# Kernel tuning notes

Hardware: AMD Instinct MI355X
Metric: run time of the kernel (lower is better)

## Reference

```python
import jax, jax.numpy as jnp
import numpy as np

B, C, H, W = 8, 64, 48, 48
W_SCALE = 0.05  # ~1/sqrt(fan_in=128)


def conv1x1(x, w, b):
    # x: [B, Cin, H, W], w: [Cout, Cin], b: [Cout]
    return jnp.einsum('oc,bchw->bohw', w, x) + b[None, :, None, None]


def setup_inputs() -> dict:
    key = jax.random.key(0)
    ks = jax.random.split(key, 12)
    n = lambda k, s, sc=1.0: jax.random.normal(k, s, dtype=jnp.float32) * sc
    return {
        'xlh': n(ks[0], (B, C, H, W)),
        'xll': n(ks[1], (B, C, H, W)),
        'xrh': n(ks[2], (B, C, H, W)),
        'xrl': n(ks[3], (B, C, H, W)),
        'concaL_w': n(ks[4], (C, 2 * C), W_SCALE), 'concaL_b': jnp.zeros((C,), jnp.float32),
        'concaR_w': n(ks[5], (C, 2 * C), W_SCALE), 'concaR_b': jnp.zeros((C,), jnp.float32),
        'gateL_w': n(ks[6], (1, C), W_SCALE), 'gateL_b': jnp.zeros((1,), jnp.float32),
        'gateR_w': n(ks[7], (1, C), W_SCALE), 'gateR_b': jnp.zeros((1,), jnp.float32),
        'concaLo_w': n(ks[8], (C, 2 * C), W_SCALE), 'concaLo_b': jnp.zeros((C,), jnp.float32),
        'concaRo_w': n(ks[9], (C, 2 * C), W_SCALE), 'concaRo_b': jnp.zeros((C,), jnp.float32),
    }


def reference(xlh, xll, xrh, xrl,
              concaL_w, concaL_b, concaR_w, concaR_b,
              gateL_w, gateL_b, gateR_w, gateR_b,
              concaLo_w, concaLo_b, concaRo_w, concaRo_b):
    xL = conv1x1(jnp.concatenate([xlh, xll], axis=1), concaL_w, concaL_b)  # [B,C,H,W]
    xR = conv1x1(jnp.concatenate([xrh, xrl], axis=1), concaR_w, concaR_b)
    bs, ch, hei, wei = xL.shape
    hw = hei * wei
    xLr = xL.reshape(bs, ch, hw)  # [B,C,HW]
    xRr = xR.reshape(bs, ch, hw)
    # Affinity = xL^T xR : [B, HW_L, HW_R]
    aff = jnp.einsum('bcn,bcm->bnm', xLr, xRr)
    a1 = jax.nn.softmax(aff, axis=1)  # softmax over left positions
    a2 = jax.nn.softmax(aff, axis=2)  # softmax over right positions
    # Branch1: xL @ a1 -> [B,C,HW]
    b1 = jnp.einsum('bcn,bnm->bcm', xLr, a1).reshape(bs, ch, hei, wei)
    g1 = jax.nn.sigmoid(conv1x1(b1, gateL_w, gateL_b))  # [B,1,H,W]
    b1 = b1 * g1
    # Branch2: xR @ a2 -> [B,C,HW]
    b2 = jnp.einsum('bcn,bnm->bcm', xRr, a2).reshape(bs, ch, hei, wei)
    g2 = jax.nn.sigmoid(conv1x1(b2, gateR_w, gateR_b))
    b2 = b2 * g2
    out_L = conv1x1(jnp.concatenate([xL, b1], axis=1), concaLo_w, concaLo_b)
    out_R = conv1x1(jnp.concatenate([xR, b2], axis=1), concaRo_w, concaRo_b)
    return (out_L, out_R)
```

## Files before the change

### kernel.cpp

```cpp
#include <hip/hip_runtime.h>

typedef unsigned short u16;
typedef __bf16 bf16_t;
typedef bf16_t bf16x8 __attribute__((ext_vector_type(8)));
typedef float f32x4 __attribute__((ext_vector_type(4)));

#define B_   8
#define CH   64
#define HW   2304
#define L2E  1.4426950408889634f

#define OFF_XLC   0u
#define OFF_XRC   2359296u
#define OFF_XLT   4718592u
#define OFF_XRT   7077888u
#define OFF_B1    9437184u
#define OFF_B2    14155776u
#define OFF_RS2   18874368u

__device__ __forceinline__ float bf2f(u16 u){
  union { unsigned int i; float f; } v; v.i = ((unsigned int)u) << 16; return v.f;
}
__device__ __forceinline__ u16 f2bf(float f){
  union { float f; unsigned int i; } v; v.f = f;
  unsigned int r = v.i + 0x7FFFu + ((v.i >> 16) & 1u);
  return (u16)(r >> 16);
}
__device__ __forceinline__ void gload16(const void* g, void* l){
  __builtin_amdgcn_global_load_lds(
      (const __attribute__((address_space(1))) void*)g,
      (__attribute__((address_space(3))) void*)l, 16, 0, 0);
}

__global__ __launch_bounds__(256) void k_proj(
    const float* xlh, const float* xll, const float* xrh, const float* xrl,
    const float* wLl, const float* bLl, const float* wRr, const float* bRr,
    char* ws)
{
  int bid = blockIdx.x;
  int b   = bid & 7;
  int q   = bid >> 3;
  int o0  = (q & 3) * 16;
  int side= (q >> 2) & 1;
  int p   = (q >> 3) * 256 + threadIdx.x;
  const float* xh = (side ? xrh : xlh) + (size_t)b*CH*HW;
  const float* xl = (side ? xrl : xll) + (size_t)b*CH*HW;
  const float* w  = (side ? wRr : wLl);
  const float* bi = (side ? bRr : bLl);

  float acc[16];
  #pragma unroll
  for (int j=0;j<16;j++) acc[j] = bi[o0+j];
  for (int c=0;c<64;c++){
    float xv = xh[(size_t)c*HW + p];
    #pragma unroll
    for (int j=0;j<16;j++) acc[j] = fmaf(w[(size_t)(o0+j)*128 + c], xv, acc[j]);
  }
  for (int c=0;c<64;c++){
    float xv = xl[(size_t)c*HW + p];
    #pragma unroll
    for (int j=0;j<16;j++) acc[j] = fmaf(w[(size_t)(o0+j)*128 + 64 + c], xv, acc[j]);
  }
  u16* xc = (u16*)(ws + (side ? OFF_XRC : OFF_XLC)) + (size_t)b*CH*HW;
  u16* xt = (u16*)(ws + (side ? OFF_XRT : OFF_XLT)) + (size_t)b*HW*CH;
  unsigned int pk[8];
  #pragma unroll
  for (int j=0;j<8;j++){
    unsigned int lo16 = f2bf(acc[2*j]);
    unsigned int hi16 = f2bf(acc[2*j+1]);
    pk[j] = lo16 | (hi16 << 16);
    xc[(size_t)(o0+2*j  )*HW + p] = (u16)lo16;
    xc[(size_t)(o0+2*j+1)*HW + p] = (u16)hi16;
  }
  uint4* dst = (uint4*)&xt[(size_t)p*CH + o0];
  dst[0] = make_uint4(pk[0],pk[1],pk[2],pk[3]);
  dst[1] = make_uint4(pk[4],pk[5],pk[6],pk[7]);
}

__global__ __launch_bounds__(256, 4) void k_stats(char* ws)
{
  __shared__ alignas(16) char smraw[16384];
  __shared__ float part[4][2][4][4];
  int bid = blockIdx.x;
  int b   = bid & 7;
  int r0  = (bid >> 3) * 32;
  const char* Xb = ws + OFF_XLT + (size_t)b*HW*CH*2;
  const char* Yb = ws + OFF_XRT + (size_t)b*HW*CH*2;
  float* out = (float*)(ws + OFF_RS2) + b*HW;

  int lane = threadIdx.x & 63;
  int wv   = __builtin_amdgcn_readfirstlane(threadIdx.x >> 6);
  int lo = lane & 15, g = lane >> 4;
  int l = lane;

  const u16* Xu = (const u16*)Xb;
  bf16x8 aA0 = *(const bf16x8*)&Xu[(size_t)(r0+lo)*CH + 8*g];
  bf16x8 aA1 = *(const bf16x8*)&Xu[(size_t)(r0+lo)*CH + 32 + 8*g];
  bf16x8 aB0 = *(const bf16x8*)&Xu[(size_t)(r0+16+lo)*CH + 8*g];
  bf16x8 aB1 = *(const bf16x8*)&Xu[(size_t)(r0+16+lo)*CH + 32 + 8*g];

  int ySrc[2];
  #pragma unroll
  for (int j=0;j<2;j++){
    int r = j*8 + (l>>3);
    ySrc[j] = r*128 + (((l&7) ^ (r&7)))*16;
  }
  char* myY = smraw + wv*4096;
  int jbP = wv*576, jbQ = jbP + 288;

  int rdP0 = lo*128 + ((g      ^ (lo&7)))*16;
  int rdP1 = lo*128 + (((4|g)  ^ (lo&7)))*16;

  #define STAGE_S(i) do { \
    const char* gp = Yb + (size_t)(jbP + (i)*16)*128; \
    const char* gq = Yb + (size_t)(jbQ + (i)*16)*128; \
    gload16(gp + ySrc[0], myY + 0);    gload16(gp + ySrc[1], myY + 1024); \
    gload16(gq + ySrc[0], myY + 2048); gload16(gq + ySrc[1], myY + 3072); \
  } while(0)

  float sPA[4] = {0.f,0.f,0.f,0.f};
  float sQA[4] = {0.f,0.f,0.f,0.f};
  float sPB[4] = {0.f,0.f,0.f,0.f};
  float sQB[4] = {0.f,0.f,0.f,0.f};

  STAGE_S(0);
  for (int i = 0; i < 18; ++i){
    asm volatile("s_waitcnt vmcnt(0)" ::: "memory");
    __builtin_amdgcn_sched_barrier(0);
    bf16x8 bP0 = *(const bf16x8*)(myY + rdP0);
    bf16x8 bP1 = *(const bf16x8*)(myY + rdP1);
    bf16x8 bQ0 = *(const bf16x8*)(myY + 2048 + rdP0);
    bf16x8 bQ1 = *(const bf16x8*)(myY + 2048 + rdP1);
    asm volatile("s_waitcnt lgkmcnt(0)" ::: "memory");
    __builtin_amdgcn_sched_barrier(0);
    int inext = (i+1 < 18) ? i+1 : 0;
    STAGE_S(inext);
    __builtin_amdgcn_sched_barrier(0);
    f32x4 z4 = {0.f,0.f,0.f,0.f};
    f32x4 dPA = __builtin_amdgcn_mfma_f32_16x16x32_bf16(aA0, bP0, z4, 0,0,0);
    dPA = __builtin_amdgcn_mfma_f32_16x16x32_bf16(aA1, bP1, dPA, 0,0,0);
    f32x4 dQA = __builtin_amdgcn_mfma_f32_16x16x32_bf16(aA0, bQ0, z4, 0,0,0);
    dQA = __builtin_amdgcn_mfma_f32_16x16x32_bf16(aA1, bQ1, dQA, 0,0,0);
    f32x4 dPB = __builtin_amdgcn_mfma_f32_16x16x32_bf16(aB0, bP0, z4, 0,0,0);
    dPB = __builtin_amdgcn_mfma_f32_16x16x32_bf16(aB1, bP1, dPB, 0,0,0);
    f32x4 dQB = __builtin_amdgcn_mfma_f32_16x16x32_bf16(aB0, bQ0, z4, 0,0,0);
    dQB = __builtin_amdgcn_mfma_f32_16x16x32_bf16(aB1, bQ1, dQB, 0,0,0);
    #pragma unroll
    for (int r=0;r<4;r++){
      sPA[r] += exp2f(dPA[r]*L2E); sQA[r] += exp2f(dQA[r]*L2E);
      sPB[r] += exp2f(dPB[r]*L2E); sQB[r] += exp2f(dQB[r]*L2E);
    }
  }
  #undef STAGE_S
  float sA[4], sB[4];
  #pragma unroll
  for (int r=0;r<4;r++){ sA[r] = sPA[r] + sQA[r]; sB[r] = sPB[r] + sQB[r]; }
  #pragma unroll
  for (int mask = 1; mask < 16; mask <<= 1){
    #pragma unroll
    for (int r=0;r<4;r++){
      sA[r] += __shfl_xor(sA[r], mask, 64);
      sB[r] += __shfl_xor(sB[r], mask, 64);
    }
  }
  if (lo == 0){
    #pragma unroll
    for (int r=0;r<4;r++){ part[wv][0][g][r] = sA[r]; part[wv][1][g][r] = sB[r]; }
  }
  __syncthreads();
  if (threadIdx.x < 32){
    int t = threadIdx.x;
    int half = t >> 4, gg = (t & 15) >> 2, rr = t & 3;
    float sum = part[0][half][gg][rr] + part[1][half][gg][rr]
              + part[2][half][gg][rr] + part[3][half][gg][rr];
    out[r0 + 16*half + 4*gg + rr] = 1.0f / sum;
  }
}

__global__ __launch_bounds__(256, 3) void k_attn(char* ws)
{
  __shared__ alignas(16) char smraw[49152];
  int bid  = blockIdx.x;
  int b    = bid & 7;
  int m0   = (bid >> 3) * 32;
  int lane = threadIdx.x & 63;
  int wv   = __builtin_amdgcn_readfirstlane(threadIdx.x >> 6);
  int lo = lane & 15, g = lane >> 4;
  int l = lane;

  const char* XLt = ws + OFF_XLT + (size_t)b*HW*CH*2;
  const char* XRt = ws + OFF_XRT + (size_t)b*HW*CH*2;
  const char* XLc = ws + OFF_XLC + (size_t)b*CH*HW*2;
  const char* XRc = ws + OFF_XRC + (size_t)b*CH*HW*2;
  const float* rs2 = (const float*)(ws + OFF_RS2) + b*HW;

  const u16* XRtu = (const u16*)XRt;
  bf16x8 fmA0 = *(const bf16x8*)&XRtu[(size_t)(m0+lo)*CH + 8*g];
  bf16x8 fmA1 = *(const bf16x8*)&XRtu[(size_t)(m0+lo)*CH + 32 + 8*g];
  bf16x8 fmB0 = *(const bf16x8*)&XRtu[(size_t)(m0+16+lo)*CH + 8*g];
  bf16x8 fmB1 = *(const bf16x8*)&XRtu[(size_t)(m0+16+lo)*CH + 32 + 8*g];

  int aSrc[4], bSrc[4];
  #pragma unroll
  for (int j=0;j<4;j++){
    int r  = j*8 + (l>>3);
    int sa = (r&3) | (((r>>3)&1)<<2);
    aSrc[j] = r*128 + (((l&7) ^ sa))*16;
    int c  = j*16 + (l>>2);
    int sb = (c>>1)&3;
    bSrc[j] = c*(HW*2) + (((l&3) ^ sb))*16;
  }
  char* myA  = smraw + wv*12288;
  char* myBL = myA + 4096;
  char* myBR = myA + 8192;

  int pr  = ((lo>>2)<<3) + (lo&3);
  int sAr = (lo&3) | (((lo>>2)&1)<<2);
  int rdA00 = pr*128     + ((g     ^ sAr))*16;
  int rdA01 = pr*128     + (((4|g) ^ sAr))*16;
  int rdA10 = (pr+4)*128 + ((g     ^ sAr))*16;
  int rdA11 = (pr+4)*128 + (((4|g) ^ sAr))*16;
  int sBr = (lo>>1)&3;
  int rdB0 = (     lo)*64 + ((g ^ sBr))*16;
  int rdB1 = (16 + lo)*64 + ((g ^ sBr))*16;
  int rdB2 = (32 + lo)*64 + ((g ^ sBr))*16;
  int rdB3 = (48 + lo)*64 + ((g ^ sBr))*16;

  #define STAGE_A(n0v) do { \
    const char* gA = XLt + (size_t)(n0v)*128; \
    const char* gL = XLc + (size_t)(n0v)*2; \
    const char* gR = XRc + (size_t)(n0v)*2; \
    gload16(gA + aSrc[0], myA  + 0);    gload16(gA + aSrc[1], myA  + 1024); \
    gload16(gA + aSrc[2], myA  + 2048); gload16(gA + aSrc[3], myA  + 3072); \
    gload16(gL + bSrc[0], myBL + 0);    gload16(gL + bSrc[1], myBL + 1024); \
    gload16(gL + bSrc[2], myBL + 2048); gload16(gL + bSrc[3], myBL + 3072); \
    gload16(gR + bSrc[0], myBR + 0);    gload16(gR + bSrc[1], myBR + 1024); \
    gload16(gR + bSrc[2], myBR + 2048); gload16(gR + bSrc[3], myBR + 3072); \
  } while(0)

  f32x4 acc1A[4], acc2A[4], acc1B[4], acc2B[4];
  #pragma unroll
  for (int ct=0;ct<4;ct++){
    f32x4 z4 = {0.f,0.f,0.f,0.f};
    acc1A[ct]=z4; acc2A[ct]=z4; acc1B[ct]=z4; acc2B[ct]=z4;
  }
  float s1A = 0.f, s1B = 0.f;

  int nbeg = wv * 576;
  STAGE_A(nbeg);
  for (int s = 0; s < 18; ++s){
    int n0 = nbeg + s*32;
    asm volatile("s_waitcnt vmcnt(0)" ::: "memory");
    __builtin_amdgcn_sched_barrier(0);
    bf16x8 fa00 = *(const bf16x8*)(myA + rdA00);
    bf16x8 fa01 = *(const bf16x8*)(myA + rdA01);
    bf16x8 fa10 = *(const bf16x8*)(myA + rdA10);
    bf16x8 fa11 = *(const bf16x8*)(myA + rdA11);
    bf16x8 bL0 = *(const bf16x8*)(myBL + rdB0);
    bf16x8 bL1 = *(const bf16x8*)(myBL + rdB1);
    bf16x8 bL2 = *(const bf16x8*)(myBL + rdB2);
    bf16x8 bL3 = *(const bf16x8*)(myBL + rdB3);
    bf16x8 bR0 = *(const bf16x8*)(myBR + rdB0);
    bf16x8 bR1 = *(const bf16x8*)(myBR + rdB1);
    bf16x8 bR2 = *(const bf16x8*)(myBR + rdB2);
    bf16x8 bR3 = *(const bf16x8*)(myBR + rdB3);
    f32x4 r20 = *(const f32x4*)&rs2[n0 + 8*g];
    f32x4 r21 = *(const f32x4*)&rs2[n0 + 8*g + 4];
    asm volatile("s_waitcnt lgkmcnt(0)" ::: "memory");
    __builtin_amdgcn_sched_barrier(0);
    int n1 = (s+1 < 18) ? n0 + 32 : nbeg;
    STAGE_A(n1);
    __builtin_amdgcn_sched_barrier(0);

    f32x4 z4 = {0.f,0.f,0.f,0.f};
    f32x4 d0A = __builtin_amdgcn_mfma_f32_16x16x32_bf16(fa00, fmA0, z4, 0,0,0);
    d0A = __builtin_amdgcn_mfma_f32_16x16x32_bf16(fa01, fmA1, d0A, 0,0,0);
    f32x4 d1A = __builtin_amdgcn_mfma_f32_16x16x32_bf16(fa10, fmA0, z4, 0,0,0);
    d1A = __builtin_amdgcn_mfma_f32_16x16x32_bf16(fa11, fmA1, d1A, 0,0,0);
    f32x4 d0B = __builtin_amdgcn_mfma_f32_16x16x32_bf16(fa00, fmB0, z4, 0,0,0);
    d0B = __builtin_amdgcn_mfma_f32_16x16x32_bf16(fa01, fmB1, d0B, 0,0,0);
    f32x4 d1B = __builtin_amdgcn_mfma_f32_16x16x32_bf16(fa10, fmB0, z4, 0,0,0);
    d1B = __builtin_amdgcn_mfma_f32_16x16x32_bf16(fa11, fmB1, d1B, 0,0,0);

    bf16x8 pa1A, pa2A, pa1B, pa2B;
    #pragma unroll
    for (int r=0;r<4;r++){
      float e0 = exp2f(d0A[r]*L2E);
      float e1 = exp2f(d1A[r]*L2E);
      s1A += e0 + e1;
      pa1A[r]   = (bf16_t)e0;
      pa1A[r+4] = (bf16_t)e1;
      pa2A[r]   = (bf16_t)(e0 * r20[r]);
      pa2A[r+4] = (bf16_t)(e1 * r21[r]);
      float f0 = exp2f(d0B[r]*L2E);
      float f1 = exp2f(d1B[r]*L2E);
      s1B += f0 + f1;
      pa1B[r]   = (bf16_t)f0;
      pa1B[r+4] = (bf16_t)f1;
      pa2B[r]   = (bf16_t)(f0 * r20[r]);
      pa2B[r+4] = (bf16_t)(f1 * r21[r]);
    }
    acc1A[0] = __builtin_amdgcn_mfma_f32_16x16x32_bf16(pa1A, bL0, acc1A[0], 0,0,0);
    acc1A[1] = __builtin_amdgcn_mfma_f32_16x16x32_bf16(pa1A, bL1, acc1A[1], 0,0,0);
    acc1A[2] = __builtin_amdgcn_mfma_f32_16x16x32_bf16(pa1A, bL2, acc1A[2], 0,0,0);
    acc1A[3] = __builtin_amdgcn_mfma_f32_16x16x32_bf16(pa1A, bL3, acc1A[3], 0,0,0);
    acc2A[0] = __builtin_amdgcn_mfma_f32_16x16x32_bf16(pa2A, bR0, acc2A[0], 0,0,0);
    acc2A[1] = __builtin_amdgcn_mfma_f32_16x16x32_bf16(pa2A, bR1, acc2A[1], 0,0,0);
    acc2A[2] = __builtin_amdgcn_mfma_f32_16x16x32_bf16(pa2A, bR2, acc2A[2], 0,0,0);
    acc2A[3] = __builtin_amdgcn_mfma_f32_16x16x32_bf16(pa2A, bR3, acc2A[3], 0,0,0);
    acc1B[0] = __builtin_amdgcn_mfma_f32_16x16x32_bf16(pa1B, bL0, acc1B[0], 0,0,0);
    acc1B[1] = __builtin_amdgcn_mfma_f32_16x16x32_bf16(pa1B, bL1, acc1B[1], 0,0,0);
    acc1B[2] = __builtin_amdgcn_mfma_f32_16x16x32_bf16(pa1B, bL2, acc1B[2], 0,0,0);
    acc1B[3] = __builtin_amdgcn_mfma_f32_16x16x32_bf16(pa1B, bL3, acc1B[3], 0,0,0);
    acc2B[0] = __builtin_amdgcn_mfma_f32_16x16x32_bf16(pa2B, bR0, acc2B[0], 0,0,0);
    acc2B[1] = __builtin_amdgcn_mfma_f32_16x16x32_bf16(pa2B, bR1, acc2B[1], 0,0,0);
    acc2B[2] = __builtin_amdgcn_mfma_f32_16x16x32_bf16(pa2B, bR2, acc2B[2], 0,0,0);
    acc2B[3] = __builtin_amdgcn_mfma_f32_16x16x32_bf16(pa2B, bR3, acc2B[3], 0,0,0);
  }
  #undef STAGE_A

  asm volatile("s_waitcnt vmcnt(0)" ::: "memory");
  __syncthreads();

  float (*red)[64][17] = (float (*)[64][17])smraw;
  float (*s1part)[32]  = (float (*)[32])(smraw + 17408);
  float* rs1inv        = (float*)(smraw + 17920);

  float s1Ar = s1A + __shfl_xor(s1A, 16, 64);
  s1Ar += __shfl_xor(s1Ar, 32, 64);
  float s1Br = s1B + __shfl_xor(s1B, 16, 64);
  s1Br += __shfl_xor(s1Br, 32, 64);
  if (lane < 16){ s1part[wv][lane] = s1Ar; s1part[wv][16+lane] = s1Br; }
  __syncthreads();
  if (threadIdx.x < 32){
    int t = threadIdx.x;
    float s = s1part[0][t] + s1part[1][t] + s1part[2][t] + s1part[3][t];
    rs1inv[t] = 1.0f / s;
  }
  __syncthreads();

  float* B1 = (float*)(ws + OFF_B1) + (size_t)b*CH*HW;
  float* B2 = (float*)(ws + OFF_B2) + (size_t)b*CH*HW;
  int tt = threadIdx.x;

  #define RED_WRITE(DST, MBASE, SCALE) do { \
    _Pragma("unroll") \
    for (int pass=0; pass<4; ++pass){ \
      int c  = (tt>>4) + pass*16; \
      int mm = tt & 15; \
      int v  = ((c>>4)<<2) + (mm&3); \
      int ll = (c&15) + ((mm>>2)<<4); \
      float s = red[0][ll][v] + red[1][ll][v] + red[2][ll][v] + red[3][ll][v]; \
      DST[(size_t)c*HW + m0 + (MBASE) + mm] = s * (SCALE); \
    } \
  } while(0)

  #pragma unroll
  for (int v=0; v<16; ++v) red[wv][lane][v] = acc1A[v>>2][v&3];
  __syncthreads();
  RED_WRITE(B1, 0, rs1inv[tt & 15]);
  __syncthreads();
  #pragma unroll
  for (int v=0; v<16; ++v) red[wv][lane][v] = acc2A[v>>2][v&3];
  __syncthreads();
  RED_WRITE(B2, 0, 1.0f);
  __syncthreads();
  #pragma unroll
  for (int v=0; v<16; ++v) red[wv][lane][v] = acc1B[v>>2][v&3];
  __syncthreads();
  RED_WRITE(B1, 16, rs1inv[16 + (tt & 15)]);
  __syncthreads();
  #pragma unroll
  for (int v=0; v<16; ++v) red[wv][lane][v] = acc2B[v>>2][v&3];
  __syncthreads();
  RED_WRITE(B2, 16, 1.0f);
  #undef RED_WRITE
}

__global__ __launch_bounds__(256) void k_out(
    char* ws,
    const float* gwL, const float* gbL, const float* gwR, const float* gbR,
    const float* wLo, const float* bLoi, const float* wRo, const float* bRoi,
    float* out)
{
  __shared__ float xT[64][64];
  __shared__ float bT[64][64];
  __shared__ float gpart[4][64];
  __shared__ float gLds[64];
  int bid = blockIdx.x;
  int b   = bid & 7;
  int q   = bid >> 3;
  int side= q & 1;
  int p0  = (q >> 1) * 64;
  int t = threadIdx.x;
  const float* braw = (const float*)(ws + (side ? OFF_B2 : OFF_B1)) + (size_t)b*CH*HW;
  const u16*   xc   = (const u16*)(ws + (side ? OFF_XRC : OFF_XLC)) + (size_t)b*CH*HW;
  const float* w    = side ? wRo : wLo;
  const float* gw   = side ? gwR : gwL;
  float        gb   = side ? gbR[0] : gbL[0];
  const float* bias = side ? bRoi : bLoi;

  #pragma unroll
  for (int i=0;i<16;i++){
    int flat = i*256 + t;
    int c = flat >> 6, pl = flat & 63;
    bT[c][pl] = braw[(size_t)c*HW + p0 + pl];
    xT[c][pl] = bf2f(xc[(size_t)c*HW + p0 + pl]);
  }
  __syncthreads();
  {
    int qq = t >> 6, pl = t & 63;
    float a = 0.f;
    #pragma unroll
    for (int c = 0; c < 16; c++) a = fmaf(gw[16*qq + c], bT[16*qq + c][pl], a);
    gpart[qq][pl] = a;
  }
  __syncthreads();
  if (t < 64){
    float x = gpart[0][t]+gpart[1][t]+gpart[2][t]+gpart[3][t] + gb;
    gLds[t] = 1.0f/(1.0f + exp2f(-x*L2E));
  }
  __syncthreads();
  #pragma unroll
  for (int i=0;i<16;i++){
    int flat = i*256 + t;
    int c = flat >> 6, pl = flat & 63;
    bT[c][pl] *= gLds[pl];
  }
  __syncthreads();
  int wv = t >> 6;
  int lane = t & 63;
  float* outp = out + ((size_t)side*B_ + b)*CH*HW;

  float acc[16];
  #pragma unroll
  for (int oi=0;oi<16;oi++) acc[oi] = bias[wv*16 + oi];
  for (int c=0;c<64;c++){
    float xv = xT[c][lane];
    float bv = bT[c][lane];
    #pragma unroll
    for (int oi=0;oi<16;oi++){
      int o = wv*16 + oi;
      acc[oi] = fmaf(w[(size_t)o*128 + c],      xv, acc[oi]);
      acc[oi] = fmaf(w[(size_t)o*128 + 64 + c], bv, acc[oi]);
    }
  }
  #pragma unroll
  for (int oi=0;oi<16;oi++){
    int o = wv*16 + oi;
    outp[(size_t)o*HW + p0 + lane] = acc[oi];
  }
}

extern "C" void kernel_launch(void* const* d_in, const int* in_sizes, int n_in,
                              void* d_out, int out_size, void* d_ws, size_t ws_size,
                              hipStream_t stream)
{
  char* ws = (char*)d_ws;
  k_proj <<<576, 256, 0, stream>>>(
      (const float*)d_in[0], (const float*)d_in[1],
      (const float*)d_in[2], (const float*)d_in[3],
      (const float*)d_in[4], (const float*)d_in[5],
      (const float*)d_in[6], (const float*)d_in[7], ws);
  k_stats<<<576, 256, 0, stream>>>(ws);
  k_attn <<<576, 256, 0, stream>>>(ws);
  k_out  <<<576, 256, 0, stream>>>(
      ws,
      (const float*)d_in[8],  (const float*)d_in[9],
      (const float*)d_in[10], (const float*)d_in[11],
      (const float*)d_in[12], (const float*)d_in[13],
      (const float*)d_in[14], (const float*)d_in[15],
      (float*)d_out);
}
```

Measured before the change: 158.7 us.

## Fuse gating and output projection into attention kernel epilogue

The separate k_out kernel is folded into the end of k_attn. The reduced branch outputs (b1, b2) now stay in shared memory instead of being written to and re-read from the workspace as fp32. The epilogue loads the matching xL/xR bf16 tile, computes the sigmoid gates, and runs both 1x1 output convolutions per 32-position tile, splitting the channels across half-waves that are combined with a shuffle. This removes one launch and the fp32 round-trip of B1/B2. In exchange the attention kernel's tail gets longer and heavier in registers: each thread holds 64 floats and reads weights scalar-per-lane, the gate dot product runs on only 64 threads, and occupancy may suffer.

```diff
diff --git a/kernel.cpp b/kernel.cpp
--- a/kernel.cpp
+++ b/kernel.cpp
@@ -14,8 +14,6 @@
 #define OFF_XRC   2359296u
 #define OFF_XLT   4718592u
 #define OFF_XRT   7077888u
-#define OFF_B1    9437184u
-#define OFF_B2    14155776u
 #define OFF_RS2   18874368u
 
 __device__ __forceinline__ float bf2f(u16 u){
@@ -177,7 +175,11 @@
   }
 }
 
-__global__ __launch_bounds__(256, 3) void k_attn(char* ws)
+__global__ __launch_bounds__(256, 3) void k_attn(
+    char* ws,
+    const float* gwL, const float* gbL, const float* gwR, const float* gbR,
+    const float* wLo, const float* bLo, const float* wRo, const float* bRo,
+    float* outp)
 {
   __shared__ alignas(16) char smraw[49152];
   int bid  = blockIdx.x;
@@ -322,9 +324,26 @@
   asm volatile("s_waitcnt vmcnt(0)" ::: "memory");
   __syncthreads();
 
-  float (*red)[64][17] = (float (*)[64][17])smraw;
-  float (*s1part)[32]  = (float (*)[32])(smraw + 17408);
-  float* rs1inv        = (float*)(smraw + 17920);
+  float (*bT1)[33]     = (float (*)[33])smraw;
+  float (*bT2)[33]     = (float (*)[33])(smraw + 8448);
+  float (*red)[64][17] = (float (*)[64][17])(smraw + 16896);
+  u16   (*xT1)[34]     = (u16 (*)[34])(smraw + 34304);
+  u16   (*xT2)[34]     = (u16 (*)[34])(smraw + 38656);
+  float (*s1part)[32]  = (float (*)[32])(smraw + 43008);
+  float* rs1inv        = (float*)(smraw + 43520);
+  float* gate          = (float*)(smraw + 43648);
+
+  int tt = threadIdx.x;
+
+  const u16* XLcu = (const u16*)XLc;
+  const u16* XRcu = (const u16*)XRc;
+  #pragma unroll
+  for (int i=0;i<8;i++){
+    int flat = i*256 + tt;
+    int c = flat >> 5, mm = flat & 31;
+    xT1[c][mm] = XLcu[(size_t)c*HW + m0 + mm];
+    xT2[c][mm] = XRcu[(size_t)c*HW + m0 + mm];
+  }
 
   float s1Ar = s1A + __shfl_xor(s1A, 16, 64);
   s1Ar += __shfl_xor(s1Ar, 32, 64);
@@ -332,18 +351,13 @@
   s1Br += __shfl_xor(s1Br, 32, 64);
   if (lane < 16){ s1part[wv][lane] = s1Ar; s1part[wv][16+lane] = s1Br; }
   __syncthreads();
-  if (threadIdx.x < 32){
-    int t = threadIdx.x;
-    float s = s1part[0][t] + s1part[1][t] + s1part[2][t] + s1part[3][t];
-    rs1inv[t] = 1.0f / s;
-  }
-  __syncthreads();
-
-  float* B1 = (float*)(ws + OFF_B1) + (size_t)b*CH*HW;
-  float* B2 = (float*)(ws + OFF_B2) + (size_t)b*CH*HW;
-  int tt = threadIdx.x;
-
-  #define RED_WRITE(DST, MBASE, SCALE) do { \
+  if (tt < 32){
+    float s = s1part[0][tt] + s1part[1][tt] + s1part[2][tt] + s1part[3][tt];
+    rs1inv[tt] = 1.0f / s;
+  }
+  __syncthreads();
+
+  #define RED_TO(DSTARR, MBASE, SCALED) do { \
     _Pragma("unroll") \
     for (int pass=0; pass<4; ++pass){ \
       int c  = (tt>>4) + pass*16; \
@@ -351,104 +365,81 @@
       int v  = ((c>>4)<<2) + (mm&3); \
       int ll = (c&15) + ((mm>>2)<<4); \
       float s = red[0][ll][v] + red[1][ll][v] + red[2][ll][v] + red[3][ll][v]; \
-      DST[(size_t)c*HW + m0 + (MBASE) + mm] = s * (SCALE); \
+      DSTARR[c][(MBASE)+mm] = (SCALED) ? s * rs1inv[(MBASE)+mm] : s; \
     } \
   } while(0)
 
   #pragma unroll
   for (int v=0; v<16; ++v) red[wv][lane][v] = acc1A[v>>2][v&3];
   __syncthreads();
-  RED_WRITE(B1, 0, rs1inv[tt & 15]);
+  RED_TO(bT1, 0, 1);
   __syncthreads();
   #pragma unroll
   for (int v=0; v<16; ++v) red[wv][lane][v] = acc2A[v>>2][v&3];
   __syncthreads();
-  RED_WRITE(B2, 0, 1.0f);
+  RED_TO(bT2, 0, 0);
   __syncthreads();
   #pragma unroll
   for (int v=0; v<16; ++v) red[wv][lane][v] = acc1B[v>>2][v&3];
   __syncthreads();
-  RED_WRITE(B1, 16, rs1inv[16 + (tt & 15)]);
+  RED_TO(bT1, 16, 1);
   __syncthreads();
   #pragma unroll
   for (int v=0; v<16; ++v) red[wv][lane][v] = acc2B[v>>2][v&3];
   __syncthreads();
-  RED_WRITE(B2, 16, 1.0f);
-  #undef RED_WRITE
-}
-
-__global__ __launch_bounds__(256) void k_out(
-    char* ws,
-    const float* gwL, const float* gbL, const float* gwR, const float* gbR,
-    const float* wLo, const float* bLoi, const float* wRo, const float* bRoi,
-    float* out)
-{
-  __shared__ float xT[64][64];
-  __shared__ float bT[64][64];
-  __shared__ float gpart[4][64];
-  __shared__ float gLds[64];
-  int bid = blockIdx.x;
-  int b   = bid & 7;
-  int q   = bid >> 3;
-  int side= q & 1;
-  int p0  = (q >> 1) * 64;
-  int t = threadIdx.x;
-  const float* braw = (const float*)(ws + (side ? OFF_B2 : OFF_B1)) + (size_t)b*CH*HW;
-  const u16*   xc   = (const u16*)(ws + (side ? OFF_XRC : OFF_XLC)) + (size_t)b*CH*HW;
-  const float* w    = side ? wRo : wLo;
-  const float* gw   = side ? gwR : gwL;
-  float        gb   = side ? gbR[0] : gbL[0];
-  const float* bias = side ? bRoi : bLoi;
-
-  #pragma unroll
-  for (int i=0;i<16;i++){
-    int flat = i*256 + t;
-    int c = flat >> 6, pl = flat & 63;
-    bT[c][pl] = braw[(size_t)c*HW + p0 + pl];
-    xT[c][pl] = bf2f(xc[(size_t)c*HW + p0 + pl]);
-  }
-  __syncthreads();
+  RED_TO(bT2, 16, 0);
+  #undef RED_TO
+  __syncthreads();
+
+  if (tt < 64){
+    int mm = tt & 31;
+    float a = 0.f;
+    if (tt < 32){
+      for (int c=0;c<64;c++) a = fmaf(gwL[c], bT1[c][mm], a);
+      gate[tt] = 1.0f/(1.0f + exp2f(-(a + gbL[0])*L2E));
+    } else {
+      for (int c=0;c<64;c++) a = fmaf(gwR[c], bT2[c][mm], a);
+      gate[tt] = 1.0f/(1.0f + exp2f(-(a + gbR[0])*L2E));
+    }
+  }
+  __syncthreads();
+  #pragma unroll
+  for (int i=0;i<8;i++){
+    int flat = i*256 + tt;
+    int c = flat >> 5, mm = flat & 31;
+    bT1[c][mm] *= gate[mm];
+    bT2[c][mm] *= gate[32+mm];
+  }
+  __syncthreads();
+
   {
-    int qq = t >> 6, pl = t & 63;
-    float a = 0.f;
-    #pragma unroll
-    for (int c = 0; c < 16; c++) a = fmaf(gw[16*qq + c], bT[16*qq + c][pl], a);
-    gpart[qq][pl] = a;
-  }
-  __syncthreads();
-  if (t < 64){
-    float x = gpart[0][t]+gpart[1][t]+gpart[2][t]+gpart[3][t] + gb;
-    gLds[t] = 1.0f/(1.0f + exp2f(-x*L2E));
-  }
-  __syncthreads();
-  #pragma unroll
-  for (int i=0;i<16;i++){
-    int flat = i*256 + t;
-    int c = flat >> 6, pl = flat & 63;
-    bT[c][pl] *= gLds[pl];
-  }
-  __syncthreads();
-  int wv = t >> 6;
-  int lane = t & 63;
-  float* outp = out + ((size_t)side*B_ + b)*CH*HW;
-
-  float acc[16];
-  #pragma unroll
-  for (int oi=0;oi<16;oi++) acc[oi] = bias[wv*16 + oi];
-  for (int c=0;c<64;c++){
-    float xv = xT[c][lane];
-    float bv = bT[c][lane];
-    #pragma unroll
-    for (int oi=0;oi<16;oi++){
-      int o = wv*16 + oi;
-      acc[oi] = fmaf(w[(size_t)o*128 + c],      xv, acc[oi]);
-      acc[oi] = fmaf(w[(size_t)o*128 + 64 + c], bv, acc[oi]);
-    }
-  }
-  #pragma unroll
-  for (int oi=0;oi<16;oi++){
-    int o = wv*16 + oi;
-    outp[(size_t)o*HW + p0 + lane] = acc[oi];
+    int side = wv >> 1;
+    int ob   = (wv & 1) * 32;
+    int mm   = lane & 31;
+    int ch   = lane >> 5;
+    const float* w    = side ? wRo : wLo;
+    const float* bias = side ? bRo : bLo;
+    float* outs = outp + ((size_t)side*B_ + b)*CH*HW;
+
+    float xr[32], br[32];
+    if (side == 0){
+      #pragma unroll
+      for (int cc=0;cc<32;cc++){ xr[cc] = bf2f(xT1[ch*32+cc][mm]); br[cc] = bT1[ch*32+cc][mm]; }
+    } else {
+      #pragma unroll
+      for (int cc=0;cc<32;cc++){ xr[cc] = bf2f(xT2[ch*32+cc][mm]); br[cc] = bT2[ch*32+cc][mm]; }
+    }
+    for (int oi=0; oi<32; ++oi){
+      int o = ob + oi;
+      const float* wr = &w[(size_t)o*128 + ch*32];
+      float a = 0.f;
+      #pragma unroll
+      for (int cc=0;cc<32;cc++) a = fmaf(wr[cc],      xr[cc], a);
+      #pragma unroll
+      for (int cc=0;cc<32;cc++) a = fmaf(wr[64+cc],   br[cc], a);
+      a += __shfl_xor(a, 32, 64);
+      if (lane < 32) outs[(size_t)o*HW + m0 + mm] = a + bias[o];
+    }
   }
 }
 
@@ -463,8 +454,7 @@
       (const float*)d_in[4], (const float*)d_in[5],
       (const float*)d_in[6], (const float*)d_in[7], ws);
   k_stats<<<576, 256, 0, stream>>>(ws);
-  k_attn <<<576, 256, 0, stream>>>(ws);
-  k_out  <<<576, 256, 0, stream>>>(
+  k_attn <<<576, 256, 0, stream>>>(
       ws,
       (const float*)d_in[8],  (const float*)d_in[9],
       (const float*)d_in[10], (const float*)d_in[11],
```

Result: faster. 150.2 us (-5.3%).
